# Optimization experiments

Measured on AMD Instinct MI355X. Metric: run time of the kernel, lower is better.

Reference implementation:

```python
import jax, jax.numpy as jnp
import numpy as np

B, T, C = 4, 2048, 1024

def setup_inputs() -> dict:
    key = jax.random.key(0)
    kx, kq, kk, kv = jax.random.split(key, 4)
    s = C ** -0.5  # match nn.Linear init scale roughly
    return {
        "x": jax.random.normal(kx, (B, T, C), dtype=jnp.float32),
        "Wq": jax.random.normal(kq, (C, C), dtype=jnp.float32) * s,
        "Wk": jax.random.normal(kk, (C, C), dtype=jnp.float32) * s,
        "Wv": jax.random.normal(kv, (C, C), dtype=jnp.float32) * s,
    }

def reference(x, Wq, Wk, Wv):
    Bq, Tq, Cq = x.shape
    # nn.Linear: y = x @ W^T (bias=False)
    q = jnp.einsum('btc,dc->btd', x, Wq)
    k = jnp.einsum('btc,dc->btd', x, Wk)
    v = jnp.einsum('btc,dc->btd', x, Wv)
    scale = Cq ** -0.5
    qk = jnp.einsum('btd,bsd->bts', q, k) * scale  # [B, T, T]
    causal = jnp.tril(jnp.ones((Tq, Tq), dtype=bool))
    qk = jnp.where(causal, qk, -jnp.inf)
    attn = jax.nn.softmax(qk, axis=-1)
    out = jnp.einsum('bts,bsd->btd', attn, v)
    return out
```

## Files before the change

kernel.cpp:

```cpp
#include <hip/hip_runtime.h>
#include <hip/hip_fp16.h>


typedef __attribute__((ext_vector_type(8))) _Float16 half8;
typedef __attribute__((ext_vector_type(4))) _Float16 half4;
typedef __attribute__((ext_vector_type(4))) float f32x4;

template<int TM, int TN, int WM, int WN, bool SWAP>
__device__ __forceinline__ void gemm_nt_core(
    const _Float16* __restrict__ A, const _Float16* __restrict__ B,
    int lda, int ldb, int k0, int k1,
    _Float16* ldsA, _Float16* ldsB,
    f32x4 acc[TM / (WM * 16)][TN / (WN * 16)])
{
    constexpr int FM = TM / (WM * 16), FN = TN / (WN * 16);
    constexpr int NA = TM / 32, NB = TN / 32;
    const int t    = threadIdx.x;
    const int lane = t & 63;
    const int w    = t >> 6;
    const int wm   = w % WM;
    const int wn   = w / WM;
    const int lr   = lane & 15;
    const int lq   = lane >> 4;

    const _Float16* ga[NA]; int loA[NA];
    const _Float16* gb[NB]; int loB[NB];
#pragma unroll
    for (int i = 0; i < NA; ++i) {
        int f = t + 256 * i;
        int r = f >> 3, c = (f & 7) ^ ((f >> 3) & 7);
        ga[i] = A + (size_t)r * lda + c * 8;
        loA[i] = f * 8;
    }
#pragma unroll
    for (int i = 0; i < NB; ++i) {
        int f = t + 256 * i;
        int r = f >> 3, c = (f & 7) ^ ((f >> 3) & 7);
        gb[i] = B + (size_t)r * ldb + c * 8;
        loB[i] = f * 8;
    }

    int offA[2][FM], offB[2][FN];
#pragma unroll
    for (int h = 0; h < 2; ++h) {
#pragma unroll
        for (int i = 0; i < FM; ++i) {
            int R = wm * (TM / WM) + i * 16 + lr;
            offA[h][i] = (8 * R + ((h * 4 + lq) ^ (R & 7))) * 8;
        }
#pragma unroll
        for (int i = 0; i < FN; ++i) {
            int R = wn * (TN / WN) + i * 16 + lr;
            offB[h][i] = (8 * R + ((h * 4 + lq) ^ (R & 7))) * 8;
        }
    }

    half8 va[NA], vb[NB];
#pragma unroll
    for (int i = 0; i < NA; ++i) va[i] = *(const half8*)(ga[i] + k0);
#pragma unroll
    for (int i = 0; i < NB; ++i) vb[i] = *(const half8*)(gb[i] + k0);

    for (int k = k0; k < k1; k += 64) {
        __syncthreads();
#pragma unroll
        for (int i = 0; i < NA; ++i) *(half8*)(ldsA + loA[i]) = va[i];
#pragma unroll
        for (int i = 0; i < NB; ++i) *(half8*)(ldsB + loB[i]) = vb[i];
        if (k + 64 < k1) {
#pragma unroll
            for (int i = 0; i < NA; ++i) va[i] = *(const half8*)(ga[i] + k + 64);
#pragma unroll
            for (int i = 0; i < NB; ++i) vb[i] = *(const half8*)(gb[i] + k + 64);
        }
        __syncthreads();

#pragma unroll
        for (int h = 0; h < 2; ++h) {
            half8 af[FM], bf[FN];
#pragma unroll
            for (int i = 0; i < FM; ++i) af[i] = *(const half8*)(ldsA + offA[h][i]);
#pragma unroll
            for (int i = 0; i < FN; ++i) bf[i] = *(const half8*)(ldsB + offB[h][i]);
#pragma unroll
            for (int mi = 0; mi < FM; ++mi)
#pragma unroll
                for (int ni = 0; ni < FN; ++ni) {
                    if constexpr (SWAP)
                        acc[mi][ni] = __builtin_amdgcn_mfma_f32_16x16x32_f16(
                            bf[ni], af[mi], acc[mi][ni], 0, 0, 0);
                    else
                        acc[mi][ni] = __builtin_amdgcn_mfma_f32_16x16x32_f16(
                            af[mi], bf[ni], acc[mi][ni], 0, 0, 0);
                }
        }
    }
}

__device__ __forceinline__ void gload_lds16(const void* g, void* l)
{
    __builtin_amdgcn_global_load_lds(
        (const __attribute__((address_space(1))) void*)g,
        (__attribute__((address_space(3))) void*)l, 16, 0, 0);
}

template<bool SWAP>
__device__ __forceinline__ void gemm_nt_256(
    const _Float16* __restrict__ A, const _Float16* __restrict__ B,
    const int lda, const int ldb, const int kTiles,
    _Float16* lds, f32x4 acc[8][4])
{
    const int t    = threadIdx.x;
    const int lane = t & 63;
    const int w    = t >> 6;
    const int wm   = w & 1;
    const int wn   = w >> 1;
    const int lr   = lane & 15;
    const int lq   = lane >> 4;

    const int r0 = t >> 3;
    const int c0 = (t & 7) ^ (r0 & 7);
    const _Float16* gA = A + (size_t)r0 * lda + c0 * 8;
    const _Float16* gB = B + (size_t)r0 * ldb + c0 * 8;

    char* ldsc = (char*)lds;
    char* stA = ldsc + w * 1024;
    char* stB = ldsc + 65536 + w * 1024;

    const int x0 = ((0 + lq) ^ (lr & 7)) * 16;
    const int x1 = ((4 + lq) ^ (lr & 7)) * 16;
    const char* rdA = ldsc + wm * 16384 + lr * 128;
    const char* rdB = ldsc + 65536 + (wn >> 1) * 16384 + (wn & 1) * 8192
                      + lr * 128;

    half8 af[4][2], bf0[2][2], bf1[2][2];

#define STGA(BUF, H, KOFF) do {                                               \
    const _Float16* _s = gA + (size_t)(H) * 128 * lda + (KOFF);               \
    char* _d = stA + (BUF) * 32768 + (H) * 16384;                             \
    gload_lds16(_s, _d);                                                      \
    gload_lds16(_s + (size_t)64 * lda, _d + 8192);                            \
} while (0)

#define STGB(BUF, H, KOFF) do {                                               \
    const _Float16* _s = gB + (size_t)(H) * 128 * ldb + (KOFF);               \
    char* _d = stB + (BUF) * 32768 + (H) * 16384;                             \
    gload_lds16(_s, _d);                                                      \
    gload_lds16(_s + (size_t)64 * ldb, _d + 8192);                            \
} while (0)

#define LDA_Q(BUF, MQ) do {                                                   \
    const char* _p = rdA + (BUF) * 32768 + (MQ) * 8192;                       \
    _Pragma("unroll")                                                         \
    for (int mi = 0; mi < 4; ++mi) {                                          \
        af[mi][0] = *(const half8*)(_p + mi * 2048 + x0);                     \
        af[mi][1] = *(const half8*)(_p + mi * 2048 + x1);                     \
    }                                                                         \
} while (0)

#define LDB_Q(DST, BUF, NQ) do {                                              \
    const char* _p = rdB + (BUF) * 32768 + (NQ) * 4096;                       \
    _Pragma("unroll")                                                         \
    for (int ni = 0; ni < 2; ++ni) {                                          \
        DST[ni][0] = *(const half8*)(_p + ni * 2048 + x0);                    \
        DST[ni][1] = *(const half8*)(_p + ni * 2048 + x1);                    \
    }                                                                         \
} while (0)

#define MFMA_Q(MQ, NQ, BSRC) do {                                             \
    _Pragma("unroll")                                                         \
    for (int mi = 0; mi < 4; ++mi)                                            \
    _Pragma("unroll")                                                         \
    for (int ni = 0; ni < 2; ++ni)                                            \
    _Pragma("unroll")                                                         \
    for (int kh = 0; kh < 2; ++kh) {                                          \
        if constexpr (SWAP)                                                   \
            acc[(MQ)*4+mi][(NQ)*2+ni] = __builtin_amdgcn_mfma_f32_16x16x32_f16(\
                BSRC[ni][kh], af[mi][kh], acc[(MQ)*4+mi][(NQ)*2+ni], 0, 0, 0);\
        else                                                                  \
            acc[(MQ)*4+mi][(NQ)*2+ni] = __builtin_amdgcn_mfma_f32_16x16x32_f16(\
                af[mi][kh], BSRC[ni][kh], acc[(MQ)*4+mi][(NQ)*2+ni], 0, 0, 0);\
    }                                                                         \
} while (0)

#define PH_PRE() do {                                                         \
    asm volatile("" ::: "memory");                                            \
    __builtin_amdgcn_s_barrier();                                             \
    asm volatile("s_waitcnt lgkmcnt(0)" ::: "memory");                        \
    __builtin_amdgcn_sched_barrier(0);                                        \
    __builtin_amdgcn_s_setprio(1);                                            \
} while (0)

#define PH_POST() do {                                                        \
    __builtin_amdgcn_s_setprio(0);                                            \
    __builtin_amdgcn_sched_barrier(0);                                        \
    __builtin_amdgcn_s_barrier();                                             \
    asm volatile("" ::: "memory");                                            \
} while (0)

#define KTILE(KT, BUF) do {                                                   \
    const int _k1 = ((KT) + 1) * 64, _k2 = ((KT) + 2) * 64;                   \
    const bool _s1 = (KT) + 1 < kTiles, _s2 = (KT) + 2 < kTiles;              \
                                                                      \
    LDA_Q(BUF, 0);                                                            \
    LDB_Q(bf0, BUF, 0);                                                       \
    if (_s1) STGA((BUF) ^ 1, 1, _k1);                                         \
    PH_PRE(); MFMA_Q(0, 0, bf0); PH_POST();                                   \
                                                                      \
    LDB_Q(bf1, BUF, 1);                                                       \
    if (_s1) STGB((BUF) ^ 1, 1, _k1);                                         \
    PH_PRE(); MFMA_Q(0, 1, bf1); PH_POST();                                   \
                                                                      \
    LDA_Q(BUF, 1);                                                            \
    if (_s2) STGB(BUF, 0, _k2);                                               \
    PH_PRE(); MFMA_Q(1, 1, bf1); PH_POST();                                   \
                                     \
    if (_s2) STGA(BUF, 0, _k2);                                               \
    asm volatile("" ::: "memory");                                            \
    __builtin_amdgcn_s_barrier();                                             \
    __builtin_amdgcn_s_setprio(1);                                            \
    MFMA_Q(1, 0, bf0);                                                        \
    __builtin_amdgcn_s_setprio(0);                                            \
    if (_s2) asm volatile("s_waitcnt vmcnt(4)" ::: "memory");                 \
    else     asm volatile("s_waitcnt vmcnt(0)" ::: "memory");                 \
    __builtin_amdgcn_sched_barrier(0);                                        \
    __builtin_amdgcn_s_barrier();                                             \
    asm volatile("" ::: "memory");                                            \
} while (0)

    STGA(0, 0, 0); STGA(0, 1, 0); STGB(0, 0, 0); STGB(0, 1, 0);
    if (kTiles > 1) { STGB(1, 0, 64); STGA(1, 0, 64); }
    if (kTiles > 1) asm volatile("s_waitcnt vmcnt(4)" ::: "memory");
    else            asm volatile("s_waitcnt vmcnt(0)" ::: "memory");
    __builtin_amdgcn_sched_barrier(0);
    __builtin_amdgcn_s_barrier();
    asm volatile("" ::: "memory");

#pragma unroll 1
    for (int kt = 0; kt < kTiles; kt += 2) {
        KTILE(kt, 0);
        KTILE(kt + 1, 1);
    }

#undef STGA
#undef STGB
#undef LDA_Q
#undef LDB_Q
#undef MFMA_Q
#undef PH_PRE
#undef PH_POST
#undef KTILE
}

__global__ __launch_bounds__(256) void f32tof16_k(
    const float* __restrict__ in, _Float16* __restrict__ out, int n)
{
    int i = (blockIdx.x * 256 + threadIdx.x) * 4;
    if (i < n) {
        float4 f = *(const float4*)(in + i);
        half4 h = { (_Float16)f.x, (_Float16)f.y, (_Float16)f.z, (_Float16)f.w };
        *(half4*)(out + i) = h;
    }
}

__global__ __launch_bounds__(256) void wconv_k(
    const float* __restrict__ Wq, const float* __restrict__ Wk,
    const float* __restrict__ Wv, _Float16* __restrict__ out)
{
    const float* src = (blockIdx.y == 0) ? Wq : (blockIdx.y == 1) ? Wk : Wv;
    int i = (blockIdx.x * 256 + threadIdx.x) * 4;
    float4 f = *(const float4*)(src + i);
    half4 h = { (_Float16)f.x, (_Float16)f.y, (_Float16)f.z, (_Float16)f.w };
    *(half4*)(out + (size_t)blockIdx.y * 1024 * 1024 + i) = h;
}

__global__ __launch_bounds__(512, 2) void qkv_gemm256_k(
    const _Float16* __restrict__ xh, const _Float16* __restrict__ Wh,
    _Float16* __restrict__ Q, _Float16* __restrict__ K,
    _Float16* __restrict__ Vt)
{
    __shared__ __align__(16) _Float16 lds[65536];
    const int tileM = blockIdx.x * 256;
    const int tileN = blockIdx.y * 256;
    const int z     = blockIdx.z;
    const _Float16* W = Wh + (size_t)z * 1024 * 1024;

    const int lane = threadIdx.x & 63;
    const int w    = threadIdx.x >> 6;
    const int wm = w & 1, wn = w >> 1;
    const int lr = lane & 15, lq = lane >> 4;

    f32x4 acc[8][4] = {};
    if (z == 2) {
        gemm_nt_256<false>(xh + (size_t)tileM * 1024, W + (size_t)tileN * 1024,
                           1024, 1024, 16, lds, acc);
#pragma unroll
        for (int mi = 0; mi < 8; ++mi)
#pragma unroll
            for (int ni = 0; ni < 4; ++ni) {
                int m0 = tileM + wm * 128 + mi * 16 + lq * 4;
                int n  = tileN + wn * 64 + ni * 16 + lr;
                int b = m0 >> 11, tt = m0 & 2047;
                half4 h = { (_Float16)acc[mi][ni][0], (_Float16)acc[mi][ni][1],
                            (_Float16)acc[mi][ni][2], (_Float16)acc[mi][ni][3] };
                *(half4*)(Vt + (size_t)b * 2048 * 1024 + (size_t)n * 2048 + tt) = h;
            }
    } else {
        gemm_nt_256<true>(xh + (size_t)tileM * 1024, W + (size_t)tileN * 1024,
                          1024, 1024, 16, lds, acc);
        _Float16* O = (z == 0) ? Q : K;
#pragma unroll
        for (int mi = 0; mi < 8; ++mi)
#pragma unroll
            for (int ni = 0; ni < 4; ++ni) {
                int tt = tileM + wm * 128 + mi * 16 + lr;
                int d0 = tileN + wn * 64 + ni * 16 + lq * 4;
                half4 h = { (_Float16)acc[mi][ni][0], (_Float16)acc[mi][ni][1],
                            (_Float16)acc[mi][ni][2], (_Float16)acc[mi][ni][3] };
                *(half4*)(O + (size_t)tt * 1024 + d0) = h;
            }
    }
}

__global__ __launch_bounds__(256) void scores_gemm_k(
    const _Float16* __restrict__ Q, const _Float16* __restrict__ K,
    _Float16* __restrict__ S)
{
    const int ti = blockIdx.x, si = blockIdx.y;
    if (si > ti) return;
    const int tileT = ti * 128, tileS = si * 128, b = blockIdx.z;

    __shared__ __align__(16) _Float16 ldsA[128 * 64];
    __shared__ __align__(16) _Float16 ldsB[128 * 64];
    f32x4 acc[4][4] = {};
    gemm_nt_core<128, 128, 2, 2, true>(
        Q + (size_t)b * 2048 * 1024 + (size_t)tileT * 1024,
        K + (size_t)b * 2048 * 1024 + (size_t)tileS * 1024,
        1024, 1024, 0, 1024, ldsA, ldsB, acc);

    const int lane = threadIdx.x & 63;
    const int w    = threadIdx.x >> 6;
    const int wm = w & 1, wn = w >> 1;
    const int lr = lane & 15, lq = lane >> 4;
    const float scale = 0.03125f;

#pragma unroll
    for (int mi = 0; mi < 4; ++mi)
#pragma unroll
        for (int ni = 0; ni < 4; ++ni) {
            int tt = tileT + wm * 64 + mi * 16 + lr;
            int s0 = tileS + wn * 64 + ni * 16 + lq * 4;
            half4 h;
#pragma unroll
            for (int r = 0; r < 4; ++r)
                h[r] = (s0 + r <= tt) ? (_Float16)(acc[mi][ni][r] * scale)
                                      : (_Float16)0.f;
            *(half4*)(S + ((size_t)b * 2048 + tt) * 2048 + s0) = h;
        }
}

__global__ __launch_bounds__(256) void softmax_k(_Float16* __restrict__ S)
{
    const int w    = threadIdx.x >> 6;
    const int lane = threadIdx.x & 63;
    const int t    = blockIdx.x * 4 + w;
    const int b    = blockIdx.y;
    _Float16* row = S + ((size_t)b * 2048 + t) * 2048;

    float x[32];
    float mx = -1e30f;
#pragma unroll
    for (int j = 0; j < 4; ++j) {
        half8 h = *(const half8*)(row + j * 512 + lane * 8);
#pragma unroll
        for (int e = 0; e < 8; ++e) {
            int s = j * 512 + lane * 8 + e;
            float f = (s <= t) ? (float)h[e] : -1e30f;
            x[j * 8 + e] = f;
            mx = fmaxf(mx, f);
        }
    }
#pragma unroll
    for (int o = 32; o > 0; o >>= 1) mx = fmaxf(mx, __shfl_xor(mx, o));

    float sum = 0.f;
#pragma unroll
    for (int i = 0; i < 32; ++i) {
        float e = __expf(x[i] - mx);
        x[i] = e;
        sum += e;
    }
#pragma unroll
    for (int o = 32; o > 0; o >>= 1) sum += __shfl_xor(sum, o);
    const float inv = 1.0f / sum;

#pragma unroll
    for (int j = 0; j < 4; ++j) {
        half8 p;
#pragma unroll
        for (int e = 0; e < 8; ++e) p[e] = (_Float16)(x[j * 8 + e] * inv);
        *(half8*)(row + j * 512 + lane * 8) = p;
    }
}

__global__ __launch_bounds__(256) void pv_gemm_k(
    const _Float16* __restrict__ P, const _Float16* __restrict__ Vt,
    float* __restrict__ out)
{
    __shared__ __align__(16) _Float16 ldsA[128 * 64];
    __shared__ __align__(16) _Float16 ldsB[64 * 64];
    const int tileT = (15 - blockIdx.x) * 128;
    const int tileD = blockIdx.y * 64;
    const int b     = blockIdx.z;
    const int kEnd  = tileT + 128;

    f32x4 acc[4][2] = {};
    gemm_nt_core<128, 64, 2, 2, true>(
        P + ((size_t)b * 2048 + tileT) * 2048,
        Vt + (size_t)b * 1024 * 2048 + (size_t)tileD * 2048,
        2048, 2048, 0, kEnd, ldsA, ldsB, acc);

    const int lane = threadIdx.x & 63;
    const int w    = threadIdx.x >> 6;
    const int wm = w & 1, wn = w >> 1;
    const int lr = lane & 15, lq = lane >> 4;

#pragma unroll
    for (int mi = 0; mi < 4; ++mi)
#pragma unroll
        for (int ni = 0; ni < 2; ++ni) {
            int tt = tileT + wm * 64 + mi * 16 + lr;
            int d0 = tileD + wn * 32 + ni * 16 + lq * 4;
            *(f32x4*)(out + ((size_t)b * 2048 + tt) * 1024 + d0) = acc[mi][ni];
        }
}

extern "C" void kernel_launch(void* const* d_in, const int* in_sizes, int n_in,
                              void* d_out, int out_size, void* d_ws, size_t ws_size,
                              hipStream_t stream)
{
    const float* x  = (const float*)d_in[0];
    const float* Wq = (const float*)d_in[1];
    const float* Wk = (const float*)d_in[2];
    const float* Wv = (const float*)d_in[3];
    float* out = (float*)d_out;

    char* ws = (char*)d_ws;
    _Float16* xh = (_Float16*)(ws);
    _Float16* Wh = (_Float16*)(ws + (16u << 20));
    _Float16* Qh = (_Float16*)(ws + (22u << 20));
    _Float16* Kh = (_Float16*)(ws + (38u << 20));
    _Float16* Vt = (_Float16*)(ws + (54u << 20));
    _Float16* S  = (_Float16*)(ws + (70u << 20));

    f32tof16_k<<<8192, 256, 0, stream>>>(x, xh, 4 * 2048 * 1024);
    wconv_k<<<dim3(1024, 3), 256, 0, stream>>>(Wq, Wk, Wv, Wh);

    qkv_gemm256_k<<<dim3(32, 4, 3), 512, 0, stream>>>(xh, Wh, Qh, Kh, Vt);

    scores_gemm_k<<<dim3(16, 16, 4), 256, 0, stream>>>(Qh, Kh, S);
    softmax_k<<<dim3(512, 4), 256, 0, stream>>>(S);
    pv_gemm_k<<<dim3(16, 16, 4), 256, 0, stream>>>(S, Vt, out);
}
```

Before: 267.2 us.

## Shrink QKV GEMM tile to 256x128 and skip fully masked softmax chunks

The QKV projection GEMM now uses a 256x128 output tile instead of 256x256, with a 4x2 wave layout. Its global-to-LDS staging and two-phase MFMA pipeline are rewritten to match, and the grid doubles to 768 blocks. The goal is better load balance across CUs (fewer partial waves) and a smaller LDS footprint, at the cost of less operand reuse per block. Separately, the softmax kernel now skips loading, exponentiating and storing 512-column chunks that lie entirely above the causal diagonal, which cuts memory traffic and ALU work on masked regions.

```diff
diff --git a/kernel.cpp b/kernel.cpp
--- a/kernel.cpp
+++ b/kernel.cpp
@@ -105,16 +105,16 @@
 }
 
 template<bool SWAP>
-__device__ __forceinline__ void gemm_nt_256(
+__device__ __forceinline__ void gemm_nt_256x128(
     const _Float16* __restrict__ A, const _Float16* __restrict__ B,
     const int lda, const int ldb, const int kTiles,
-    _Float16* lds, f32x4 acc[8][4])
+    _Float16* lds, f32x4 acc[4][4])
 {
     const int t    = threadIdx.x;
     const int lane = t & 63;
     const int w    = t >> 6;
-    const int wm   = w & 1;
-    const int wn   = w >> 1;
+    const int wm   = w & 3;
+    const int wn   = w >> 2;
     const int lr   = lane & 15;
     const int lq   = lane >> 4;
 
@@ -129,28 +129,21 @@
 
     const int x0 = ((0 + lq) ^ (lr & 7)) * 16;
     const int x1 = ((4 + lq) ^ (lr & 7)) * 16;
-    const char* rdA = ldsc + wm * 16384 + lr * 128;
-    const char* rdB = ldsc + 65536 + (wn >> 1) * 16384 + (wn & 1) * 8192
-                      + lr * 128;
-
-    half8 af[4][2], bf0[2][2], bf1[2][2];
-
-#define STGA(BUF, H, KOFF) do {                                               \
-    const _Float16* _s = gA + (size_t)(H) * 128 * lda + (KOFF);               \
-    char* _d = stA + (BUF) * 32768 + (H) * 16384;                             \
-    gload_lds16(_s, _d);                                                      \
-    gload_lds16(_s + (size_t)64 * lda, _d + 8192);                            \
-} while (0)
-
-#define STGB(BUF, H, KOFF) do {                                               \
-    const _Float16* _s = gB + (size_t)(H) * 128 * ldb + (KOFF);               \
-    char* _d = stB + (BUF) * 32768 + (H) * 16384;                             \
-    gload_lds16(_s, _d);                                                      \
-    gload_lds16(_s + (size_t)64 * ldb, _d + 8192);                            \
-} while (0)
-
-#define LDA_Q(BUF, MQ) do {                                                   \
-    const char* _p = rdA + (BUF) * 32768 + (MQ) * 8192;                       \
+    const char* rdA = ldsc + wm * 8192 + lr * 128;
+    const char* rdB = ldsc + 65536 + wn * 8192 + lr * 128;
+
+    half8 af[4][2], bf01[2][2], bf23[2][2];
+
+#define STGA1(BUF, S, KOFF)                                                   \
+    gload_lds16(gA + (size_t)(S) * 64 * lda + (KOFF),                         \
+                stA + (BUF) * 32768 + (S) * 8192)
+
+#define STGB1(BUF, S, KOFF)                                                   \
+    gload_lds16(gB + (size_t)(S) * 64 * ldb + (KOFF),                         \
+                stB + (BUF) * 16384 + (S) * 8192)
+
+#define LDA_ALL(BUF) do {                                                     \
+    const char* _p = rdA + (BUF) * 32768;                                     \
     _Pragma("unroll")                                                         \
     for (int mi = 0; mi < 4; ++mi) {                                          \
         af[mi][0] = *(const half8*)(_p + mi * 2048 + x0);                     \
@@ -158,8 +151,8 @@
     }                                                                         \
 } while (0)
 
-#define LDB_Q(DST, BUF, NQ) do {                                              \
-    const char* _p = rdB + (BUF) * 32768 + (NQ) * 4096;                       \
+#define LDB_H(DST, BUF, NQ) do {                                              \
+    const char* _p = rdB + (BUF) * 16384 + (NQ) * 4096;                       \
     _Pragma("unroll")                                                         \
     for (int ni = 0; ni < 2; ++ni) {                                          \
         DST[ni][0] = *(const half8*)(_p + ni * 2048 + x0);                    \
@@ -167,7 +160,7 @@
     }                                                                         \
 } while (0)
 
-#define MFMA_Q(MQ, NQ, BSRC) do {                                             \
+#define MFMA_NH(NQ, BSRC) do {                                                \
     _Pragma("unroll")                                                         \
     for (int mi = 0; mi < 4; ++mi)                                            \
     _Pragma("unroll")                                                         \
@@ -175,11 +168,11 @@
     _Pragma("unroll")                                                         \
     for (int kh = 0; kh < 2; ++kh) {                                          \
         if constexpr (SWAP)                                                   \
-            acc[(MQ)*4+mi][(NQ)*2+ni] = __builtin_amdgcn_mfma_f32_16x16x32_f16(\
-                BSRC[ni][kh], af[mi][kh], acc[(MQ)*4+mi][(NQ)*2+ni], 0, 0, 0);\
+            acc[mi][(NQ)*2+ni] = __builtin_amdgcn_mfma_f32_16x16x32_f16(      \
+                BSRC[ni][kh], af[mi][kh], acc[mi][(NQ)*2+ni], 0, 0, 0);       \
         else                                                                  \
-            acc[(MQ)*4+mi][(NQ)*2+ni] = __builtin_amdgcn_mfma_f32_16x16x32_f16(\
-                af[mi][kh], BSRC[ni][kh], acc[(MQ)*4+mi][(NQ)*2+ni], 0, 0, 0);\
+            acc[mi][(NQ)*2+ni] = __builtin_amdgcn_mfma_f32_16x16x32_f16(      \
+                af[mi][kh], BSRC[ni][kh], acc[mi][(NQ)*2+ni], 0, 0, 0);       \
     }                                                                         \
 } while (0)
 
@@ -201,25 +194,21 @@
 #define KTILE(KT, BUF) do {                                                   \
     const int _k1 = ((KT) + 1) * 64, _k2 = ((KT) + 2) * 64;                   \
     const bool _s1 = (KT) + 1 < kTiles, _s2 = (KT) + 2 < kTiles;              \
-                                                                      \
-    LDA_Q(BUF, 0);                                                            \
-    LDB_Q(bf0, BUF, 0);                                                       \
-    if (_s1) STGA((BUF) ^ 1, 1, _k1);                                         \
-    PH_PRE(); MFMA_Q(0, 0, bf0); PH_POST();                                   \
-                                                                      \
-    LDB_Q(bf1, BUF, 1);                                                       \
-    if (_s1) STGB((BUF) ^ 1, 1, _k1);                                         \
-    PH_PRE(); MFMA_Q(0, 1, bf1); PH_POST();                                   \
-                                                                      \
-    LDA_Q(BUF, 1);                                                            \
-    if (_s2) STGB(BUF, 0, _k2);                                               \
-    PH_PRE(); MFMA_Q(1, 1, bf1); PH_POST();                                   \
-                                     \
-    if (_s2) STGA(BUF, 0, _k2);                                               \
+                                                                     \
+    LDA_ALL(BUF);                                                             \
+    LDB_H(bf01, BUF, 0);                                                      \
+    if (_s1) { STGB1((BUF) ^ 1, 0, _k1); STGB1((BUF) ^ 1, 1, _k1); }          \
+    PH_PRE(); MFMA_NH(0, bf01); PH_POST();                                    \
+                                                                     \
+    LDB_H(bf23, BUF, 1);                                                      \
+    if (_s2) { STGA1(BUF, 0, _k2); STGA1(BUF, 1, _k2);                        \
+               STGA1(BUF, 2, _k2); STGA1(BUF, 3, _k2); }                      \
     asm volatile("" ::: "memory");                                            \
     __builtin_amdgcn_s_barrier();                                             \
+    asm volatile("s_waitcnt lgkmcnt(0)" ::: "memory");                        \
+    __builtin_amdgcn_sched_barrier(0);                                        \
     __builtin_amdgcn_s_setprio(1);                                            \
-    MFMA_Q(1, 0, bf0);                                                        \
+    MFMA_NH(1, bf23);                                                         \
     __builtin_amdgcn_s_setprio(0);                                            \
     if (_s2) asm volatile("s_waitcnt vmcnt(4)" ::: "memory");                 \
     else     asm volatile("s_waitcnt vmcnt(0)" ::: "memory");                 \
@@ -228,8 +217,10 @@
     asm volatile("" ::: "memory");                                            \
 } while (0)
 
-    STGA(0, 0, 0); STGA(0, 1, 0); STGB(0, 0, 0); STGB(0, 1, 0);
-    if (kTiles > 1) { STGB(1, 0, 64); STGA(1, 0, 64); }
+    STGA1(0, 0, 0); STGA1(0, 1, 0); STGA1(0, 2, 0); STGA1(0, 3, 0);
+    STGB1(0, 0, 0); STGB1(0, 1, 0);
+    if (kTiles > 1) { STGA1(1, 0, 64); STGA1(1, 1, 64);
+                      STGA1(1, 2, 64); STGA1(1, 3, 64); }
     if (kTiles > 1) asm volatile("s_waitcnt vmcnt(4)" ::: "memory");
     else            asm volatile("s_waitcnt vmcnt(0)" ::: "memory");
     __builtin_amdgcn_sched_barrier(0);
@@ -242,11 +233,11 @@
         KTILE(kt + 1, 1);
     }
 
-#undef STGA
-#undef STGB
-#undef LDA_Q
-#undef LDB_Q
-#undef MFMA_Q
+#undef STGA1
+#undef STGB1
+#undef LDA_ALL
+#undef LDB_H
+#undef MFMA_NH
 #undef PH_PRE
 #undef PH_POST
 #undef KTILE
@@ -279,26 +270,27 @@
     _Float16* __restrict__ Q, _Float16* __restrict__ K,
     _Float16* __restrict__ Vt)
 {
-    __shared__ __align__(16) _Float16 lds[65536];
+    __shared__ __align__(16) _Float16 lds[49152];
     const int tileM = blockIdx.x * 256;
-    const int tileN = blockIdx.y * 256;
+    const int tileN = blockIdx.y * 128;
     const int z     = blockIdx.z;
     const _Float16* W = Wh + (size_t)z * 1024 * 1024;
 
     const int lane = threadIdx.x & 63;
     const int w    = threadIdx.x >> 6;
-    const int wm = w & 1, wn = w >> 1;
+    const int wm = w & 3, wn = w >> 2;
     const int lr = lane & 15, lq = lane >> 4;
 
-    f32x4 acc[8][4] = {};
+    f32x4 acc[4][4] = {};
     if (z == 2) {
-        gemm_nt_256<false>(xh + (size_t)tileM * 1024, W + (size_t)tileN * 1024,
-                           1024, 1024, 16, lds, acc);
-#pragma unroll
-        for (int mi = 0; mi < 8; ++mi)
+        gemm_nt_256x128<false>(xh + (size_t)tileM * 1024,
+                               W + (size_t)tileN * 1024,
+                               1024, 1024, 16, lds, acc);
+#pragma unroll
+        for (int mi = 0; mi < 4; ++mi)
 #pragma unroll
             for (int ni = 0; ni < 4; ++ni) {
-                int m0 = tileM + wm * 128 + mi * 16 + lq * 4;
+                int m0 = tileM + wm * 64 + mi * 16 + lq * 4;
                 int n  = tileN + wn * 64 + ni * 16 + lr;
                 int b = m0 >> 11, tt = m0 & 2047;
                 half4 h = { (_Float16)acc[mi][ni][0], (_Float16)acc[mi][ni][1],
@@ -306,14 +298,15 @@
                 *(half4*)(Vt + (size_t)b * 2048 * 1024 + (size_t)n * 2048 + tt) = h;
             }
     } else {
-        gemm_nt_256<true>(xh + (size_t)tileM * 1024, W + (size_t)tileN * 1024,
-                          1024, 1024, 16, lds, acc);
+        gemm_nt_256x128<true>(xh + (size_t)tileM * 1024,
+                              W + (size_t)tileN * 1024,
+                              1024, 1024, 16, lds, acc);
         _Float16* O = (z == 0) ? Q : K;
 #pragma unroll
-        for (int mi = 0; mi < 8; ++mi)
+        for (int mi = 0; mi < 4; ++mi)
 #pragma unroll
             for (int ni = 0; ni < 4; ++ni) {
-                int tt = tileM + wm * 128 + mi * 16 + lr;
+                int tt = tileM + wm * 64 + mi * 16 + lr;
                 int d0 = tileN + wn * 64 + ni * 16 + lq * 4;
                 half4 h = { (_Float16)acc[mi][ni][0], (_Float16)acc[mi][ni][1],
                             (_Float16)acc[mi][ni][2], (_Float16)acc[mi][ni][3] };
@@ -366,18 +359,21 @@
     const int t    = blockIdx.x * 4 + w;
     const int b    = blockIdx.y;
     _Float16* row = S + ((size_t)b * 2048 + t) * 2048;
+    const int jmax = t >> 9;
 
     float x[32];
     float mx = -1e30f;
 #pragma unroll
     for (int j = 0; j < 4; ++j) {
-        half8 h = *(const half8*)(row + j * 512 + lane * 8);
-#pragma unroll
-        for (int e = 0; e < 8; ++e) {
-            int s = j * 512 + lane * 8 + e;
-            float f = (s <= t) ? (float)h[e] : -1e30f;
-            x[j * 8 + e] = f;
-            mx = fmaxf(mx, f);
+        if (j <= jmax) {
+            half8 h = *(const half8*)(row + j * 512 + lane * 8);
+#pragma unroll
+            for (int e = 0; e < 8; ++e) {
+                int s = j * 512 + lane * 8 + e;
+                float f = (s <= t) ? (float)h[e] : -1e30f;
+                x[j * 8 + e] = f;
+                mx = fmaxf(mx, f);
+            }
         }
     }
 #pragma unroll
@@ -385,10 +381,15 @@
 
     float sum = 0.f;
 #pragma unroll
-    for (int i = 0; i < 32; ++i) {
-        float e = __expf(x[i] - mx);
-        x[i] = e;
-        sum += e;
+    for (int j = 0; j < 4; ++j) {
+        if (j <= jmax) {
+#pragma unroll
+            for (int e = 0; e < 8; ++e) {
+                float ex = __expf(x[j * 8 + e] - mx);
+                x[j * 8 + e] = ex;
+                sum += ex;
+            }
+        }
     }
 #pragma unroll
     for (int o = 32; o > 0; o >>= 1) sum += __shfl_xor(sum, o);
@@ -396,10 +397,12 @@
 
 #pragma unroll
     for (int j = 0; j < 4; ++j) {
-        half8 p;
-#pragma unroll
-        for (int e = 0; e < 8; ++e) p[e] = (_Float16)(x[j * 8 + e] * inv);
-        *(half8*)(row + j * 512 + lane * 8) = p;
+        if (j <= jmax) {
+            half8 p;
+#pragma unroll
+            for (int e = 0; e < 8; ++e) p[e] = (_Float16)(x[j * 8 + e] * inv);
+            *(half8*)(row + j * 512 + lane * 8) = p;
+        }
     }
 }
 
@@ -456,7 +459,7 @@
     f32tof16_k<<<8192, 256, 0, stream>>>(x, xh, 4 * 2048 * 1024);
     wconv_k<<<dim3(1024, 3), 256, 0, stream>>>(Wq, Wk, Wv, Wh);
 
-    qkv_gemm256_k<<<dim3(32, 4, 3), 512, 0, stream>>>(xh, Wh, Qh, Kh, Vt);
+    qkv_gemm256_k<<<dim3(32, 8, 3), 512, 0, stream>>>(xh, Wh, Qh, Kh, Vt);
 
     scores_gemm_k<<<dim3(16, 16, 4), 256, 0, stream>>>(Qh, Kh, S);
     softmax_k<<<dim3(512, 4), 256, 0, stream>>>(S);
```

Result: faster. 249.0 us (-6.8%).
